# Kernel tuning notes

Hardware: AMD Instinct MI355X
Metric: run time of the kernel (lower is better)

The kernel has to match this reference:

```python
import jax, jax.numpy as jnp
import numpy as np

B, T, C = 64, 256, 384
H = 6
D = C // H  # head_size = 64


def setup_inputs() -> dict:
    key = jax.random.key(0)
    ks = jax.random.split(key, 6)
    s = 1.0 / np.sqrt(C)
    return {
        "x": jax.random.normal(ks[0], (B, T, C), dtype=jnp.float32),
        "Wk": jax.random.uniform(ks[1], (C, C), jnp.float32, -s, s),
        "Wq": jax.random.uniform(ks[2], (C, C), jnp.float32, -s, s),
        "Wv": jax.random.uniform(ks[3], (C, C), jnp.float32, -s, s),
        "Wo": jax.random.uniform(ks[4], (C, C), jnp.float32, -s, s),
        "bo": jax.random.uniform(ks[5], (C,), jnp.float32, -s, s),
    }


def reference(x, Wk, Wq, Wv, Wo, bo):
    b, t, c = x.shape
    # QKV projections (no bias), split heads: [B, H, T, D]
    k = (x @ Wk.T).reshape(b, t, H, D).transpose(0, 2, 1, 3)
    q = (x @ Wq.T).reshape(b, t, H, D).transpose(0, 2, 1, 3)
    v = (x @ Wv.T).reshape(b, t, H, D).transpose(0, 2, 1, 3)
    # Scores scaled by C**-0.5 (as in the original module, not head_size**-0.5)
    wei = jnp.einsum("bhqd,bhkd->bhqk", q, k) * (c ** -0.5)
    mask = jnp.tril(jnp.ones((t, t), dtype=bool))
    wei = jnp.where(mask, wei, -jnp.inf)
    wei = jax.nn.softmax(wei, axis=-1)
    out = jnp.einsum("bhqk,bhkd->bhqd", wei, v)
    out = out.transpose(0, 2, 1, 3).reshape(b, t, c)
    # Output projection (dropout is identity at inference)
    return out @ Wo.T + bo
```

## Files before the change

### kernel.cpp

```cpp
#include <hip/hip_runtime.h>
#include <hip/hip_bf16.h>

typedef unsigned short u16;
typedef __attribute__((ext_vector_type(8))) short short8;
typedef __attribute__((ext_vector_type(4))) float f32x4;

#define BATCH 64
#define SEQ   256
#define CDIM  384
#define NHEAD 6
#define DHEAD 64
#define NROW  16384

constexpr float SCALE = 0.051031036307982884f;

__device__ __forceinline__ f32x4 mfma16(short8 a, short8 b, f32x4 c) {
    return __builtin_amdgcn_mfma_f32_16x16x32_bf16(a, b, c, 0, 0, 0);
}

__device__ __forceinline__ u16 f2b(float f) {
    __hip_bfloat16 h = __float2bfloat16(f);
    return *reinterpret_cast<u16*>(&h);
}

__device__ __forceinline__ void gload_lds16(const u16* g, u16* l) {
    __builtin_amdgcn_global_load_lds(
        (const __attribute__((address_space(1))) void*)g,
        (__attribute__((address_space(3))) void*)l, 16, 0, 0);
}

__global__ __launch_bounds__(256) void cvt_all(
        const float* __restrict__ x,
        const float* __restrict__ Wk, const float* __restrict__ Wq,
        const float* __restrict__ Wv, const float* __restrict__ Wo,
        u16* __restrict__ xb,
        u16* __restrict__ wkb, u16* __restrict__ wqb,
        u16* __restrict__ wvb, u16* __restrict__ wob)
{
    int blk = blockIdx.x;
    const float* s;
    u16* d;
    if (blk < 3072) {
        s = x; d = xb;
    } else {
        const int w = blk - 3072;
        const int z = w / 72;
        blk = w - z * 72;
        s = (z == 0) ? Wk : (z == 1) ? Wq : (z == 2) ? Wv : Wo;
        d = (z == 0) ? wkb : (z == 1) ? wqb : (z == 2) ? wvb : wob;
    }
    const int i = (blk * 256 + threadIdx.x) * 8;
    const float4 a = *(const float4*)(s + i);
    const float4 b = *(const float4*)(s + i + 4);
    short8 r;
    r[0] = (short)f2b(a.x); r[1] = (short)f2b(a.y);
    r[2] = (short)f2b(a.z); r[3] = (short)f2b(a.w);
    r[4] = (short)f2b(b.x); r[5] = (short)f2b(b.y);
    r[6] = (short)f2b(b.z); r[7] = (short)f2b(b.w);
    *(short8*)(d + i) = r;
}

__global__ __launch_bounds__(256) void gemm_qkv(
        const u16* __restrict__ X, const u16* __restrict__ Wk,
        const u16* __restrict__ Wv, const u16* __restrict__ Wq,
        u16* __restrict__ Kd, u16* __restrict__ VTd, u16* __restrict__ Qd)
{
    __shared__ u16 SMEM[17408];
    u16* As = SMEM;
    u16* Bs = SMEM + 8192;

    const int n0 = blockIdx.x * 128;
    const int m0 = blockIdx.y * 128;
    const int z  = blockIdx.z;
    const u16* W = (z == 0) ? Wk : (z == 1 ? Wv : Wq);

    const int tid  = threadIdx.x;
    const int lane = tid & 63;
    const int wv   = tid >> 6;
    const int l15  = lane & 15;
    const int q4   = lane >> 4;
    const int wm   = (wv >> 1) * 64;
    const int wn   = (wv & 1) * 64;

    f32x4 acc[4][4] = {};

    for (int kk = 0; kk < CDIM; kk += 64) {
        __syncthreads();
#pragma unroll
        for (int ch = 0; ch < 4; ++ch) {
            const int f = (ch * 256 + tid) * 8;
            const int r = f >> 6;
            const int c = (f ^ ((r & 7) << 3)) & 63;
            const int lb = (ch * 256 + wv * 64) * 8;
            gload_lds16(X + (size_t)(m0 + r) * CDIM + kk + c, As + lb);
            gload_lds16(W + (size_t)(n0 + r) * CDIM + kk + c, Bs + lb);
        }
        __syncthreads();

#pragma unroll
        for (int ks = 0; ks < 2; ++ks) {
            short8 af[4], bf[4];
#pragma unroll
            for (int t = 0; t < 4; ++t) {
                const int ra = wm + t * 16 + l15;
                const int rb = wn + t * 16 + l15;
                af[t] = *(const short8*)(As + ra * 64 +
                        ((ks * 32 + q4 * 8) ^ ((ra & 7) << 3)));
                bf[t] = *(const short8*)(Bs + rb * 64 +
                        ((ks * 32 + q4 * 8) ^ ((rb & 7) << 3)));
            }
#pragma unroll
            for (int tm = 0; tm < 4; ++tm)
#pragma unroll
                for (int tn = 0; tn < 4; ++tn)
                    acc[tm][tn] = mfma16(af[tm], bf[tn], acc[tm][tn]);
        }
    }
    __syncthreads();

    if (z != 1) {
        u16* D = (z == 0) ? Kd : Qd;
        u16* T = SMEM;
#pragma unroll
        for (int tm = 0; tm < 4; ++tm)
#pragma unroll
            for (int tn = 0; tn < 4; ++tn) {
                const int cl = wn + tn * 16 + l15;
#pragma unroll
                for (int r = 0; r < 4; ++r) {
                    const int row = wm + tm * 16 + q4 * 4 + r;
                    T[row * 128 + (((cl >> 3) ^ (row & 7)) << 3) + (cl & 7)] =
                        f2b(acc[tm][tn][r]);
                }
            }
        __syncthreads();
        const int seg0 = tid >> 3;
        const int c    = tid & 7;
#pragma unroll
        for (int it = 0; it < 8; ++it) {
            const int S   = it * 32 + seg0;
            const int row = S >> 1;
            const int hf  = S & 1;
            const int rowg = m0 + row;
            const int b  = rowg >> 8, tt = rowg & 255;
            const int h  = (n0 + hf * 64) >> 6;
            const int chunk = (hf * 8 + c) ^ (row & 7);
            *(uint4*)(D + (size_t)((b * NHEAD + h) * SEQ + tt) * DHEAD + c * 8) =
                *(const uint4*)(T + row * 128 + chunk * 8);
        }
    } else {
        u16* T = SMEM;
#pragma unroll
        for (int tm = 0; tm < 4; ++tm)
#pragma unroll
            for (int tn = 0; tn < 4; ++tn) {
                const int cl = wn + tn * 16 + l15;
#pragma unroll
                for (int r = 0; r < 4; ++r) {
                    const int rl = wm + tm * 16 + q4 * 4 + r;
                    T[cl * 136 + rl] = f2b(acc[tm][tn][r]);
                }
            }
        __syncthreads();
        const int b  = m0 >> 8;
        const int t0 = m0 & 255;
        const int fl = tid >> 1;
        const int hf = tid & 1;
        const int fg = n0 + fl;
        const int h  = fg >> 6, d = fg & 63;
        u16* dst = VTd + ((size_t)(b * NHEAD + h) * DHEAD + d) * SEQ + t0 + hf * 64;
        const u16* src = T + fl * 136 + hf * 64;
#pragma unroll
        for (int j = 0; j < 8; ++j)
            *(uint4*)(dst + j * 8) = *(const uint4*)(src + j * 8);
    }
}

#define PLD 264

template <int CH>
__device__ __forceinline__ void attn_body(
        const u16* __restrict__ Qg, const u16* __restrict__ Kg,
        const u16* __restrict__ VTg, u16* __restrict__ Og, int bh,
        u16* SA, u16* Pbase)
{
    constexpr int NKEY = 64 * (CH + 1);
    constexpr int KT   = NKEY / 16;
    constexpr int NPH  = (NKEY + 127) / 128;

    const int tid  = threadIdx.x;
    const int wv   = tid >> 6;
    const int lane = tid & 63;
    const int l15  = lane & 15;
    const int q4   = lane >> 4;
    const int qrow0 = CH * 64 + wv * 16;
    const int qmax  = qrow0 + 15;
    u16* Pl = Pbase + wv * 16 * PLD;

    short8 aq[2];
#pragma unroll
    for (int ks = 0; ks < 2; ++ks)
        aq[ks] = *(const short8*)(Qg + (size_t)(bh * SEQ + qrow0 + l15) * DHEAD
                                     + ks * 32 + q4 * 8);

    u16* Kbuf = SA;
    f32x4 s[KT];
#pragma unroll
    for (int ph = 0; ph < NPH; ++ph) {
        const int rows = (NKEY - ph * 128) < 128 ? (NKEY - ph * 128) : 128;
        for (int it = 0; it < rows / 32; ++it) {
            const int r  = it * 32 + (tid >> 3);
            const int d0 = (tid & 7) * 8;
            *(uint4*)(Kbuf + r * 72 + d0) =
                *(const uint4*)(Kg + (size_t)(bh * SEQ + ph * 128 + r) * DHEAD + d0);
        }
        __syncthreads();
#pragma unroll
        for (int t = 0; t < rows / 16; ++t) {
            const int gt = ph * 8 + t;
            if (gt * 16 <= qmax) {
                f32x4 z = {0.f, 0.f, 0.f, 0.f};
#pragma unroll
                for (int ks = 0; ks < 2; ++ks) {
                    short8 bk = *(const short8*)(Kbuf + (t * 16 + l15) * 72
                                                 + ks * 32 + q4 * 8);
                    z = mfma16(aq[ks], bk, z);
                }
                const int kc = gt * 16 + l15;
#pragma unroll
                for (int r = 0; r < 4; ++r) {
                    float v = z[r] * SCALE;
                    if (kc > qrow0 + q4 * 4 + r) v = -1e30f;
                    z[r] = v;
                }
                s[gt] = z;
            } else {
                f32x4 neg = {-1e30f, -1e30f, -1e30f, -1e30f};
                s[gt] = neg;
            }
        }
        __syncthreads();
    }

    float mx[4], sm[4], rs[4];
#pragma unroll
    for (int r = 0; r < 4; ++r) {
        float m = -1e30f;
#pragma unroll
        for (int t = 0; t < KT; ++t) m = fmaxf(m, s[t][r]);
#pragma unroll
        for (int off = 1; off < 16; off <<= 1)
            m = fmaxf(m, __shfl_xor(m, off, 16));
        mx[r] = m;
        sm[r] = 0.f;
    }
#pragma unroll
    for (int t = 0; t < KT; ++t)
#pragma unroll
        for (int r = 0; r < 4; ++r) {
            float p = __expf(s[t][r] - mx[r]);
            s[t][r] = p;
            sm[r] += p;
        }
#pragma unroll
    for (int r = 0; r < 4; ++r) {
#pragma unroll
        for (int off = 1; off < 16; off <<= 1)
            sm[r] += __shfl_xor(sm[r], off, 16);
        rs[r] = 1.f / sm[r];
    }

#pragma unroll
    for (int gt = 0; gt < KT; ++gt)
#pragma unroll
        for (int r = 0; r < 4; ++r)
            Pl[(q4 * 4 + r) * PLD + gt * 16 + l15] = f2b(s[gt][r]);

    u16* Vt = SA;
    f32x4 o[4] = {};
#pragma unroll
    for (int ph = 0; ph < NPH; ++ph) {
        const int rows = (NKEY - ph * 128) < 128 ? (NKEY - ph * 128) : 128;
        const int cpr  = rows >> 3;
#pragma unroll
        for (int it = 0; it < 4; ++it) {
            if (it < cpr / 4) {
                const int flat = it * 256 + tid;
                const int rd = flat / cpr;
                const int kc = (flat - rd * cpr) * 8;
                *(uint4*)(Vt + rd * 136 + kc) =
                    *(const uint4*)(VTg + ((size_t)bh * DHEAD + rd) * SEQ
                                        + ph * 128 + kc);
            }
        }
        __syncthreads();
#pragma unroll
        for (int ks = 0; ks < rows / 32; ++ks) {
            const int gks = ph * 4 + ks;
            if (gks * 32 <= qmax) {
                short8 ap = *(const short8*)(Pl + l15 * PLD + gks * 32 + q4 * 8);
#pragma unroll
                for (int tn = 0; tn < 4; ++tn) {
                    short8 bv = *(const short8*)(Vt + (tn * 16 + l15) * 136
                                                 + ks * 32 + q4 * 8);
                    o[tn] = mfma16(ap, bv, o[tn]);
                }
            }
        }
        __syncthreads();
    }

    u16* OL = SA;
#pragma unroll
    for (int tn = 0; tn < 4; ++tn) {
        const int col = tn * 16 + l15;
#pragma unroll
        for (int r = 0; r < 4; ++r) {
            const int row = wv * 16 + q4 * 4 + r;
            OL[row * 64 + (((col >> 3) ^ (row & 7)) << 3) + (col & 7)] =
                f2b(o[tn][r] * rs[r]);
        }
    }
    __syncthreads();
    const int seg0 = tid >> 3;
    const int c    = tid & 7;
#pragma unroll
    for (int it = 0; it < 2; ++it) {
        const int row = it * 32 + seg0;
        const int chunk = c ^ (row & 7);
        *(uint4*)(Og + (size_t)(bh * SEQ + CH * 64 + row) * DHEAD + c * 8) =
            *(const uint4*)(OL + row * 64 + chunk * 8);
    }
}

__global__ __launch_bounds__(256) void attn_kernel(
        const u16* __restrict__ Qg, const u16* __restrict__ Kg,
        const u16* __restrict__ VTg, u16* __restrict__ Og)
{
    __shared__ u16 SA[128 * 72];
    __shared__ u16 Pls[4 * 16 * PLD];
    const int bh = blockIdx.y;
    switch (blockIdx.x) {
        case 0: attn_body<0>(Qg, Kg, VTg, Og, bh, SA, Pls); break;
        case 1: attn_body<1>(Qg, Kg, VTg, Og, bh, SA, Pls); break;
        case 2: attn_body<2>(Qg, Kg, VTg, Og, bh, SA, Pls); break;
        default: attn_body<3>(Qg, Kg, VTg, Og, bh, SA, Pls); break;
    }
}

__global__ __launch_bounds__(256) void gemm_out(
        const u16* __restrict__ O, const u16* __restrict__ Wo,
        const float* __restrict__ bias, float* __restrict__ out)
{
    __shared__ u16 As[64 * 64];
    __shared__ u16 Bs[128 * 64];

    const int n0 = blockIdx.x * 128;
    const int m0 = blockIdx.y * 64;

    const int tid  = threadIdx.x;
    const int lane = tid & 63;
    const int wv   = tid >> 6;
    const int l15  = lane & 15;
    const int q4   = lane >> 4;
    const int wm   = (wv >> 1) * 32;
    const int wn   = (wv & 1) * 64;

    f32x4 acc[2][4] = {};

    for (int kk = 0; kk < CDIM; kk += 64) {
        __syncthreads();
#pragma unroll
        for (int ch = 0; ch < 4; ++ch) {
            const int f = (ch * 256 + tid) * 8;
            const int r = f >> 6;
            const int c = (f ^ ((r & 7) << 3)) & 63;
            const int lb = (ch * 256 + wv * 64) * 8;
            gload_lds16(Wo + (size_t)(n0 + r) * CDIM + kk + c, Bs + lb);
            if (ch < 2) {
                const int row = m0 + r;
                const int b = row >> 8, t = row & 255;
                const int k = kk + c;
                const int hh = k >> 6, dd = k & 63;
                gload_lds16(O + (size_t)((b * NHEAD + hh) * SEQ + t) * DHEAD + dd,
                            As + lb);
            }
        }
        __syncthreads();

#pragma unroll
        for (int ks = 0; ks < 2; ++ks) {
            short8 af[2], bf[4];
#pragma unroll
            for (int t = 0; t < 2; ++t) {
                const int ra = wm + t * 16 + l15;
                af[t] = *(const short8*)(As + ra * 64 +
                        ((ks * 32 + q4 * 8) ^ ((ra & 7) << 3)));
            }
#pragma unroll
            for (int t = 0; t < 4; ++t) {
                const int rb = wn + t * 16 + l15;
                bf[t] = *(const short8*)(Bs + rb * 64 +
                        ((ks * 32 + q4 * 8) ^ ((rb & 7) << 3)));
            }
#pragma unroll
            for (int tm = 0; tm < 2; ++tm)
#pragma unroll
                for (int tn = 0; tn < 4; ++tn)
                    acc[tm][tn] = mfma16(af[tm], bf[tn], acc[tm][tn]);
        }
    }

#pragma unroll
    for (int tm = 0; tm < 2; ++tm) {
#pragma unroll
        for (int tn = 0; tn < 4; ++tn) {
            const int col = n0 + wn + tn * 16 + l15;
            const float bb = bias[col];
#pragma unroll
            for (int r = 0; r < 4; ++r) {
                const int row = m0 + wm + tm * 16 + q4 * 4 + r;
                out[(size_t)row * CDIM + col] = acc[tm][tn][r] + bb;
            }
        }
    }
}

extern "C" void kernel_launch(void* const* d_in, const int* in_sizes, int n_in,
                              void* d_out, int out_size, void* d_ws, size_t ws_size,
                              hipStream_t stream)
{
    const float* x  = (const float*)d_in[0];
    const float* Wk = (const float*)d_in[1];
    const float* Wq = (const float*)d_in[2];
    const float* Wv = (const float*)d_in[3];
    const float* Wo = (const float*)d_in[4];
    const float* bo = (const float*)d_in[5];
    float* out = (float*)d_out;

    const size_t SZ = (size_t)NROW * CDIM;
    const size_t WZ = (size_t)CDIM * CDIM;
    u16* xb  = (u16*)d_ws;
    u16* Wkb = xb  + SZ;
    u16* Wqb = Wkb + WZ;
    u16* Wvb = Wqb + WZ;
    u16* Wob = Wvb + WZ;
    u16* Kw  = Wob + WZ;
    u16* Qw  = Kw + SZ;
    u16* Ow  = Qw + SZ;
    u16* VTw = (u16*)d_out;

    cvt_all<<<dim3(3360), 256, 0, stream>>>(
        x, Wk, Wq, Wv, Wo, xb, Wkb, Wqb, Wvb, Wob);

    dim3 g1(CDIM / 128, NROW / 128, 3);
    gemm_qkv<<<g1, 256, 0, stream>>>(xb, Wkb, Wvb, Wqb, Kw, VTw, Qw);

    dim3 g2(4, BATCH * NHEAD);
    attn_kernel<<<g2, 256, 0, stream>>>(Qw, Kw, VTw, Ow);

    dim3 g3(CDIM / 128, NROW / 64);
    gemm_out<<<g3, 256, 0, stream>>>(Ow, Wob, bo, out);
}
```

Measured before the change: 155.8 us.

## Fuse all four stages into one persistent cooperative kernel with grid syncs

Replaces the four separate launches (convert, QKV GEMM, attention, output GEMM) with a single persistent cooperative kernel. Each stage runs as a grid-stride loop over its work items, and stages are separated by grid-wide syncs. The occupancy-sized grid (up to 3 blocks per CU over 256 CUs) is meant to remove launch overhead and inter-kernel gaps. In exchange it adds grid barrier cost, forces one shared-memory allocation sized for the largest stage (which can lower occupancy), and may leave tail imbalance per stage; the old multi-kernel path is kept as a fallback.

After: 371.6 us. 2.39x slower.

```diff
diff --git a/kernel.cpp b/kernel.cpp
--- a/kernel.cpp
+++ b/kernel.cpp
@@ -1,5 +1,8 @@
 #include <hip/hip_runtime.h>
 #include <hip/hip_bf16.h>
+#include <hip/hip_cooperative_groups.h>
+
+namespace cg = cooperative_groups;
 
 typedef unsigned short u16;
 typedef __attribute__((ext_vector_type(8))) short short8;
@@ -29,7 +32,9 @@
         (__attribute__((address_space(3))) void*)l, 16, 0, 0);
 }
 
-__global__ __launch_bounds__(256) void cvt_all(
+
+__device__ __forceinline__ void cvt_body(
+        int blk,
         const float* __restrict__ x,
         const float* __restrict__ Wk, const float* __restrict__ Wq,
         const float* __restrict__ Wv, const float* __restrict__ Wo,
@@ -37,7 +42,6 @@
         u16* __restrict__ wkb, u16* __restrict__ wqb,
         u16* __restrict__ wvb, u16* __restrict__ wob)
 {
-    int blk = blockIdx.x;
     const float* s;
     u16* d;
     if (blk < 3072) {
@@ -49,7 +53,7 @@
         s = (z == 0) ? Wk : (z == 1) ? Wq : (z == 2) ? Wv : Wo;
         d = (z == 0) ? wkb : (z == 1) ? wqb : (z == 2) ? wvb : wob;
     }
-    const int i = (blk * 256 + threadIdx.x) * 8;
+    const int i = (blk * 256 + (int)threadIdx.x) * 8;
     const float4 a = *(const float4*)(s + i);
     const float4 b = *(const float4*)(s + i + 4);
     short8 r;
@@ -60,18 +64,14 @@
     *(short8*)(d + i) = r;
 }
 
-__global__ __launch_bounds__(256) void gemm_qkv(
+__device__ __forceinline__ void qkv_body(
+        int n0, int m0, int z, u16* SMEM,
         const u16* __restrict__ X, const u16* __restrict__ Wk,
         const u16* __restrict__ Wv, const u16* __restrict__ Wq,
         u16* __restrict__ Kd, u16* __restrict__ VTd, u16* __restrict__ Qd)
 {
-    __shared__ u16 SMEM[17408];
     u16* As = SMEM;
     u16* Bs = SMEM + 8192;
-
-    const int n0 = blockIdx.x * 128;
-    const int m0 = blockIdx.y * 128;
-    const int z  = blockIdx.z;
     const u16* W = (z == 0) ? Wk : (z == 1 ? Wv : Wq);
 
     const int tid  = threadIdx.x;
@@ -333,30 +333,27 @@
     }
 }
 
-__global__ __launch_bounds__(256) void attn_kernel(
+__device__ __forceinline__ void attn_dispatch(
+        int ch, int bh,
         const u16* __restrict__ Qg, const u16* __restrict__ Kg,
-        const u16* __restrict__ VTg, u16* __restrict__ Og)
-{
-    __shared__ u16 SA[128 * 72];
-    __shared__ u16 Pls[4 * 16 * PLD];
-    const int bh = blockIdx.y;
-    switch (blockIdx.x) {
-        case 0: attn_body<0>(Qg, Kg, VTg, Og, bh, SA, Pls); break;
-        case 1: attn_body<1>(Qg, Kg, VTg, Og, bh, SA, Pls); break;
-        case 2: attn_body<2>(Qg, Kg, VTg, Og, bh, SA, Pls); break;
-        default: attn_body<3>(Qg, Kg, VTg, Og, bh, SA, Pls); break;
-    }
-}
-
-__global__ __launch_bounds__(256) void gemm_out(
+        const u16* __restrict__ VTg, u16* __restrict__ Og,
+        u16* SA, u16* Pbase)
+{
+    switch (ch) {
+        case 0: attn_body<0>(Qg, Kg, VTg, Og, bh, SA, Pbase); break;
+        case 1: attn_body<1>(Qg, Kg, VTg, Og, bh, SA, Pbase); break;
+        case 2: attn_body<2>(Qg, Kg, VTg, Og, bh, SA, Pbase); break;
+        default: attn_body<3>(Qg, Kg, VTg, Og, bh, SA, Pbase); break;
+    }
+}
+
+__device__ __forceinline__ void out_body(
+        int n0, int m0, u16* SMEM,
         const u16* __restrict__ O, const u16* __restrict__ Wo,
         const float* __restrict__ bias, float* __restrict__ out)
 {
-    __shared__ u16 As[64 * 64];
-    __shared__ u16 Bs[128 * 64];
-
-    const int n0 = blockIdx.x * 128;
-    const int m0 = blockIdx.y * 64;
+    u16* As = SMEM;
+    u16* Bs = SMEM + 4096;
 
     const int tid  = threadIdx.x;
     const int lane = tid & 63;
@@ -426,6 +423,90 @@
     }
 }
 
+#define SMEM_U16 26112
+
+__global__ __launch_bounds__(256) void mega(
+        const float* __restrict__ x,
+        const float* __restrict__ Wk, const float* __restrict__ Wq,
+        const float* __restrict__ Wv, const float* __restrict__ Wo,
+        const float* __restrict__ bo,
+        u16* xb, u16* Wkb, u16* Wqb, u16* Wvb, u16* Wob,
+        u16* Kw, u16* Qw, u16* Ow, u16* VTw, float* out)
+{
+    __shared__ u16 SMEM[SMEM_U16];
+    const int gsz = gridDim.x;
+
+    for (int wb = blockIdx.x; wb < 3360; wb += gsz)
+        cvt_body(wb, x, Wk, Wq, Wv, Wo, xb, Wkb, Wqb, Wvb, Wob);
+
+    __threadfence();
+    cg::this_grid().sync();
+
+    for (int wb = blockIdx.x; wb < 1152; wb += gsz) {
+        const int n0 = (wb % 3) * 128;
+        const int m0 = ((wb / 3) & 127) * 128;
+        const int z  = wb / 384;
+        qkv_body(n0, m0, z, SMEM, xb, Wkb, Wvb, Wqb, Kw, VTw, Qw);
+        __syncthreads();
+    }
+
+    __threadfence();
+    cg::this_grid().sync();
+
+    for (int wb = blockIdx.x; wb < 1536; wb += gsz) {
+        attn_dispatch(wb & 3, wb >> 2, Qw, Kw, VTw, Ow,
+                      SMEM, SMEM + 9216);
+        __syncthreads();
+    }
+
+    __threadfence();
+    cg::this_grid().sync();
+
+    for (int wb = blockIdx.x; wb < 768; wb += gsz) {
+        const int n0 = (wb % 3) * 128;
+        const int m0 = (wb / 3) * 64;
+        out_body(n0, m0, SMEM, Ow, Wob, bo, out);
+        __syncthreads();
+    }
+}
+
+__global__ __launch_bounds__(256) void cvt_all_k(
+        const float* __restrict__ x,
+        const float* __restrict__ Wk, const float* __restrict__ Wq,
+        const float* __restrict__ Wv, const float* __restrict__ Wo,
+        u16* __restrict__ xb, u16* __restrict__ wkb, u16* __restrict__ wqb,
+        u16* __restrict__ wvb, u16* __restrict__ wob)
+{
+    cvt_body(blockIdx.x, x, Wk, Wq, Wv, Wo, xb, wkb, wqb, wvb, wob);
+}
+
+__global__ __launch_bounds__(256) void gemm_qkv_k(
+        const u16* __restrict__ X, const u16* __restrict__ Wk,
+        const u16* __restrict__ Wv, const u16* __restrict__ Wq,
+        u16* __restrict__ Kd, u16* __restrict__ VTd, u16* __restrict__ Qd)
+{
+    __shared__ u16 SMEM[17408];
+    qkv_body(blockIdx.x * 128, blockIdx.y * 128, blockIdx.z, SMEM,
+             X, Wk, Wv, Wq, Kd, VTd, Qd);
+}
+
+__global__ __launch_bounds__(256) void attn_k(
+        const u16* __restrict__ Qg, const u16* __restrict__ Kg,
+        const u16* __restrict__ VTg, u16* __restrict__ Og)
+{
+    __shared__ u16 SA[128 * 72];
+    __shared__ u16 Pls[4 * 16 * PLD];
+    attn_dispatch(blockIdx.x, blockIdx.y, Qg, Kg, VTg, Og, SA, Pls);
+}
+
+__global__ __launch_bounds__(256) void gemm_out_k(
+        const u16* __restrict__ O, const u16* __restrict__ Wo,
+        const float* __restrict__ bias, float* __restrict__ out)
+{
+    __shared__ u16 SMEM[64 * 64 + 128 * 64];
+    out_body(blockIdx.x * 128, blockIdx.y * 64, SMEM, O, Wo, bias, out);
+}
+
 extern "C" void kernel_launch(void* const* d_in, const int* in_sizes, int n_in,
                               void* d_out, int out_size, void* d_ws, size_t ws_size,
                               hipStream_t stream)
@@ -450,15 +531,32 @@
     u16* Ow  = Qw + SZ;
     u16* VTw = (u16*)d_out;
 
-    cvt_all<<<dim3(3360), 256, 0, stream>>>(
-        x, Wk, Wq, Wv, Wo, xb, Wkb, Wqb, Wvb, Wob);
-
-    dim3 g1(CDIM / 128, NROW / 128, 3);
-    gemm_qkv<<<g1, 256, 0, stream>>>(xb, Wkb, Wvb, Wqb, Kw, VTw, Qw);
-
-    dim3 g2(4, BATCH * NHEAD);
-    attn_kernel<<<g2, 256, 0, stream>>>(Qw, Kw, VTw, Ow);
-
-    dim3 g3(CDIM / 128, NROW / 64);
-    gemm_out<<<g3, 256, 0, stream>>>(Ow, Wob, bo, out);
-}
+    static int coop_grid = -1;
+    if (coop_grid < 0) {
+        int nb = 0;
+        if (hipOccupancyMaxActiveBlocksPerMultiprocessor(&nb, mega, 256, 0)
+                != hipSuccess || nb < 1)
+            nb = 1;
+        if (nb > 3) nb = 3;
+        coop_grid = nb * 256;
+    }
+
+    void* args[] = {
+        (void*)&x, (void*)&Wk, (void*)&Wq, (void*)&Wv, (void*)&Wo, (void*)&bo,
+        (void*)&xb, (void*)&Wkb, (void*)&Wqb, (void*)&Wvb, (void*)&Wob,
+        (void*)&Kw, (void*)&Qw, (void*)&Ow, (void*)&VTw, (void*)&out };
+
+    hipError_t e = hipLaunchCooperativeKernel(
+        mega, dim3(coop_grid), dim3(256), args, 0, stream);
+
+    if (e != hipSuccess) {
+        cvt_all_k<<<dim3(3360), 256, 0, stream>>>(
+            x, Wk, Wq, Wv, Wo, xb, Wkb, Wqb, Wvb, Wob);
+        dim3 g1(CDIM / 128, NROW / 128, 3);
+        gemm_qkv_k<<<g1, 256, 0, stream>>>(xb, Wkb, Wvb, Wqb, Kw, VTw, Qw);
+        dim3 g2(4, BATCH * NHEAD);
+        attn_k<<<g2, 256, 0, stream>>>(Qw, Kw, VTw, Ow);
+        dim3 g3(CDIM / 128, NROW / 64);
+        gemm_out_k<<<g3, 256, 0, stream>>>(Ow, Wob, bo, out);
+    }
+}
```

## Fuse fp32-to-bf16 conversion into GEMM tile loads and store O token-major

Applied to the files above, without the earlier changes.

Removes the separate conversion kernel. The QKV and output GEMMs now read fp32 x and weights directly, converting to bf16 in registers before writing the swizzled LDS tiles. The attention kernel writes its output in [B,T,C] layout, so the output GEMM can load O rows contiguously. This saves one launch and the bf16 copy round trip. In exchange, the direct-to-LDS async loads become register-staged loads, and x is re-read as fp32 by each of the three N-tile blocks and the three projections.

Result: slower. 168.3 us (+8.0%).

```diff
diff --git a/kernel.cpp b/kernel.cpp
--- a/kernel.cpp
+++ b/kernel.cpp
@@ -23,46 +23,24 @@
     return *reinterpret_cast<u16*>(&h);
 }
 
-__device__ __forceinline__ void gload_lds16(const u16* g, u16* l) {
-    __builtin_amdgcn_global_load_lds(
-        (const __attribute__((address_space(1))) void*)g,
-        (__attribute__((address_space(3))) void*)l, 16, 0, 0);
-}
-
-__global__ __launch_bounds__(256) void cvt_all(
-        const float* __restrict__ x,
-        const float* __restrict__ Wk, const float* __restrict__ Wq,
-        const float* __restrict__ Wv, const float* __restrict__ Wo,
-        u16* __restrict__ xb,
-        u16* __restrict__ wkb, u16* __restrict__ wqb,
-        u16* __restrict__ wvb, u16* __restrict__ wob)
-{
-    int blk = blockIdx.x;
-    const float* s;
-    u16* d;
-    if (blk < 3072) {
-        s = x; d = xb;
-    } else {
-        const int w = blk - 3072;
-        const int z = w / 72;
-        blk = w - z * 72;
-        s = (z == 0) ? Wk : (z == 1) ? Wq : (z == 2) ? Wv : Wo;
-        d = (z == 0) ? wkb : (z == 1) ? wqb : (z == 2) ? wvb : wob;
-    }
-    const int i = (blk * 256 + threadIdx.x) * 8;
-    const float4 a = *(const float4*)(s + i);
-    const float4 b = *(const float4*)(s + i + 4);
+__device__ __forceinline__ short8 pack8(float4 a, float4 b) {
     short8 r;
     r[0] = (short)f2b(a.x); r[1] = (short)f2b(a.y);
     r[2] = (short)f2b(a.z); r[3] = (short)f2b(a.w);
     r[4] = (short)f2b(b.x); r[5] = (short)f2b(b.y);
     r[6] = (short)f2b(b.z); r[7] = (short)f2b(b.w);
-    *(short8*)(d + i) = r;
+    return r;
+}
+
+__device__ __forceinline__ void gload_lds16(const u16* g, u16* l) {
+    __builtin_amdgcn_global_load_lds(
+        (const __attribute__((address_space(1))) void*)g,
+        (__attribute__((address_space(3))) void*)l, 16, 0, 0);
 }
 
 __global__ __launch_bounds__(256) void gemm_qkv(
-        const u16* __restrict__ X, const u16* __restrict__ Wk,
-        const u16* __restrict__ Wv, const u16* __restrict__ Wq,
+        const float* __restrict__ X, const float* __restrict__ Wk,
+        const float* __restrict__ Wv, const float* __restrict__ Wq,
         u16* __restrict__ Kd, u16* __restrict__ VTd, u16* __restrict__ Qd)
 {
     __shared__ u16 SMEM[17408];
@@ -72,7 +50,7 @@
     const int n0 = blockIdx.x * 128;
     const int m0 = blockIdx.y * 128;
     const int z  = blockIdx.z;
-    const u16* W = (z == 0) ? Wk : (z == 1 ? Wv : Wq);
+    const float* W = (z == 0) ? Wk : (z == 1 ? Wv : Wq);
 
     const int tid  = threadIdx.x;
     const int lane = tid & 63;
@@ -90,10 +68,16 @@
         for (int ch = 0; ch < 4; ++ch) {
             const int f = (ch * 256 + tid) * 8;
             const int r = f >> 6;
-            const int c = (f ^ ((r & 7) << 3)) & 63;
-            const int lb = (ch * 256 + wv * 64) * 8;
-            gload_lds16(X + (size_t)(m0 + r) * CDIM + kk + c, As + lb);
-            gload_lds16(W + (size_t)(n0 + r) * CDIM + kk + c, Bs + lb);
+            const int c = f & 63;
+            const size_t gx = (size_t)(m0 + r) * CDIM + kk + c;
+            const size_t gw = (size_t)(n0 + r) * CDIM + kk + c;
+            const float4 xa = *(const float4*)(X + gx);
+            const float4 xb = *(const float4*)(X + gx + 4);
+            const float4 wa = *(const float4*)(W + gw);
+            const float4 wb = *(const float4*)(W + gw + 4);
+            const int off = r * 64 + (c ^ ((r & 7) << 3));
+            *(short8*)(As + off) = pack8(xa, xb);
+            *(short8*)(Bs + off) = pack8(wa, wb);
         }
         __syncthreads();
 
@@ -322,13 +306,16 @@
         }
     }
     __syncthreads();
+    const int b  = bh / NHEAD;
+    const int h  = bh - b * NHEAD;
     const int seg0 = tid >> 3;
     const int c    = tid & 7;
 #pragma unroll
     for (int it = 0; it < 2; ++it) {
         const int row = it * 32 + seg0;
         const int chunk = c ^ (row & 7);
-        *(uint4*)(Og + (size_t)(bh * SEQ + CH * 64 + row) * DHEAD + c * 8) =
+        *(uint4*)(Og + (size_t)(b * SEQ + CH * 64 + row) * CDIM
+                     + h * DHEAD + c * 8) =
             *(const uint4*)(OL + row * 64 + chunk * 8);
     }
 }
@@ -349,7 +336,7 @@
 }
 
 __global__ __launch_bounds__(256) void gemm_out(
-        const u16* __restrict__ O, const u16* __restrict__ Wo,
+        const u16* __restrict__ O, const float* __restrict__ Wo,
         const float* __restrict__ bias, float* __restrict__ out)
 {
     __shared__ u16 As[64 * 64];
@@ -371,20 +358,22 @@
     for (int kk = 0; kk < CDIM; kk += 64) {
         __syncthreads();
 #pragma unroll
-        for (int ch = 0; ch < 4; ++ch) {
+        for (int ch = 0; ch < 2; ++ch) {
             const int f = (ch * 256 + tid) * 8;
             const int r = f >> 6;
             const int c = (f ^ ((r & 7) << 3)) & 63;
             const int lb = (ch * 256 + wv * 64) * 8;
-            gload_lds16(Wo + (size_t)(n0 + r) * CDIM + kk + c, Bs + lb);
-            if (ch < 2) {
-                const int row = m0 + r;
-                const int b = row >> 8, t = row & 255;
-                const int k = kk + c;
-                const int hh = k >> 6, dd = k & 63;
-                gload_lds16(O + (size_t)((b * NHEAD + hh) * SEQ + t) * DHEAD + dd,
-                            As + lb);
-            }
+            gload_lds16(O + (size_t)(m0 + r) * CDIM + kk + c, As + lb);
+        }
+#pragma unroll
+        for (int ch = 0; ch < 4; ++ch) {
+            const int f = (ch * 256 + tid) * 8;
+            const int r = f >> 6;
+            const int c = f & 63;
+            const size_t gw = (size_t)(n0 + r) * CDIM + kk + c;
+            const float4 wa = *(const float4*)(Wo + gw);
+            const float4 wb = *(const float4*)(Wo + gw + 4);
+            *(short8*)(Bs + r * 64 + (c ^ ((r & 7) << 3))) = pack8(wa, wb);
         }
         __syncthreads();
 
@@ -439,26 +428,17 @@
     float* out = (float*)d_out;
 
     const size_t SZ = (size_t)NROW * CDIM;
-    const size_t WZ = (size_t)CDIM * CDIM;
-    u16* xb  = (u16*)d_ws;
-    u16* Wkb = xb  + SZ;
-    u16* Wqb = Wkb + WZ;
-    u16* Wvb = Wqb + WZ;
-    u16* Wob = Wvb + WZ;
-    u16* Kw  = Wob + WZ;
+    u16* Kw  = (u16*)d_ws;
     u16* Qw  = Kw + SZ;
     u16* Ow  = Qw + SZ;
     u16* VTw = (u16*)d_out;
 
-    cvt_all<<<dim3(3360), 256, 0, stream>>>(
-        x, Wk, Wq, Wv, Wo, xb, Wkb, Wqb, Wvb, Wob);
-
     dim3 g1(CDIM / 128, NROW / 128, 3);
-    gemm_qkv<<<g1, 256, 0, stream>>>(xb, Wkb, Wvb, Wqb, Kw, VTw, Qw);
+    gemm_qkv<<<g1, 256, 0, stream>>>(x, Wk, Wv, Wq, Kw, VTw, Qw);
 
     dim3 g2(4, BATCH * NHEAD);
     attn_kernel<<<g2, 256, 0, stream>>>(Qw, Kw, VTw, Ow);
 
     dim3 g3(CDIM / 128, NROW / 64);
-    gemm_out<<<g3, 256, 0, stream>>>(Ow, Wob, bo, out);
-}
+    gemm_out<<<g3, 256, 0, stream>>>(Ow, Wo, bo, out);
+}
```

## Swizzle QKV GEMM blocks per XCD and store attention output row-major

Applied to the files above, without the earlier changes.

The QKV GEMM launch becomes a flat 1D grid whose block index is remapped so that each XCD (block index mod 8) gets contiguous 128-row panels, and all 9 (n, z) tiles of a panel run on the same XCD. The aim is for the x panel to be reused from that XCD's L2. The attention kernel now writes its output in [B,T,C] row-major layout, so the output GEMM loads A rows contiguously instead of gathering per-head addresses. The block mapping assumes blocks are dispatched round-robin across 8 XCDs; if that assumption fails it only costs locality, not correctness.

Result: faster. 152.3 us (-2.2%).

```diff
diff --git a/kernel.cpp b/kernel.cpp
--- a/kernel.cpp
+++ b/kernel.cpp
@@ -49,7 +49,7 @@
         s = (z == 0) ? Wk : (z == 1) ? Wq : (z == 2) ? Wv : Wo;
         d = (z == 0) ? wkb : (z == 1) ? wqb : (z == 2) ? wvb : wob;
     }
-    const int i = (blk * 256 + threadIdx.x) * 8;
+    const int i = (blk * 256 + (int)threadIdx.x) * 8;
     const float4 a = *(const float4*)(s + i);
     const float4 b = *(const float4*)(s + i + 4);
     short8 r;
@@ -69,9 +69,15 @@
     u16* As = SMEM;
     u16* Bs = SMEM + 8192;
 
-    const int n0 = blockIdx.x * 128;
-    const int m0 = blockIdx.y * 128;
-    const int z  = blockIdx.z;
+    const int bid   = blockIdx.x;
+    const int xcd   = bid & 7;
+    const int i     = bid >> 3;
+    const int igrp  = i / 9;
+    const int j     = i - igrp * 9;
+    const int panel = xcd * 16 + igrp;
+    const int m0    = panel * 128;
+    const int n0    = (j % 3) * 128;
+    const int z     = j / 3;
     const u16* W = (z == 0) ? Wk : (z == 1 ? Wv : Wq);
 
     const int tid  = threadIdx.x;
@@ -171,8 +177,8 @@
         u16* dst = VTd + ((size_t)(b * NHEAD + h) * DHEAD + d) * SEQ + t0 + hf * 64;
         const u16* src = T + fl * 136 + hf * 64;
 #pragma unroll
-        for (int j = 0; j < 8; ++j)
-            *(uint4*)(dst + j * 8) = *(const uint4*)(src + j * 8);
+        for (int j2 = 0; j2 < 8; ++j2)
+            *(uint4*)(dst + j2 * 8) = *(const uint4*)(src + j2 * 8);
     }
 }
 
@@ -322,13 +328,16 @@
         }
     }
     __syncthreads();
+    const int b  = bh / NHEAD;
+    const int h  = bh - b * NHEAD;
     const int seg0 = tid >> 3;
     const int c    = tid & 7;
 #pragma unroll
     for (int it = 0; it < 2; ++it) {
         const int row = it * 32 + seg0;
         const int chunk = c ^ (row & 7);
-        *(uint4*)(Og + (size_t)(bh * SEQ + CH * 64 + row) * DHEAD + c * 8) =
+        *(uint4*)(Og + (size_t)(b * SEQ + CH * 64 + row) * CDIM
+                     + h * DHEAD + c * 8) =
             *(const uint4*)(OL + row * 64 + chunk * 8);
     }
 }
@@ -377,14 +386,8 @@
             const int c = (f ^ ((r & 7) << 3)) & 63;
             const int lb = (ch * 256 + wv * 64) * 8;
             gload_lds16(Wo + (size_t)(n0 + r) * CDIM + kk + c, Bs + lb);
-            if (ch < 2) {
-                const int row = m0 + r;
-                const int b = row >> 8, t = row & 255;
-                const int k = kk + c;
-                const int hh = k >> 6, dd = k & 63;
-                gload_lds16(O + (size_t)((b * NHEAD + hh) * SEQ + t) * DHEAD + dd,
-                            As + lb);
-            }
+            if (ch < 2)
+                gload_lds16(O + (size_t)(m0 + r) * CDIM + kk + c, As + lb);
         }
         __syncthreads();
 
@@ -453,8 +456,7 @@
     cvt_all<<<dim3(3360), 256, 0, stream>>>(
         x, Wk, Wq, Wv, Wo, xb, Wkb, Wqb, Wvb, Wob);
 
-    dim3 g1(CDIM / 128, NROW / 128, 3);
-    gemm_qkv<<<g1, 256, 0, stream>>>(xb, Wkb, Wvb, Wqb, Kw, VTw, Qw);
+    gemm_qkv<<<dim3(1152), 256, 0, stream>>>(xb, Wkb, Wvb, Wqb, Kw, VTw, Qw);
 
     dim3 g2(4, BATCH * NHEAD);
     attn_kernel<<<g2, 256, 0, stream>>>(Qw, Kw, VTw, Ow);
```
